# Performance work log

Measured on AMD Instinct MI355X. Metric: run time of the kernel, lower is better.

Reference implementation:

```python
import jax, jax.numpy as jnp
import numpy as np

B = 32768
NUM_SPARSE = 26
VOCAB = 100000
EMB = 128
DENSE_IN = 13
N_FIELDS = NUM_SPARSE + 1  # 27
INTER_DIM = N_FIELDS * (N_FIELDS - 1) // 2  # 351
TOP_IN = EMB + INTER_DIM  # 479


def setup_inputs() -> dict:
    key = jax.random.key(0)
    ks = jax.random.split(key, 12)
    inp = {
        "dense_x": jax.random.normal(ks[0], (B, DENSE_IN), dtype=jnp.float32),
        "sparse_x": jax.random.randint(ks[1], (B, NUM_SPARSE), 0, VOCAB, dtype=jnp.int64),
        # embedding tables stacked: [F, V, D]
        "emb_tables": jax.random.normal(ks[2], (NUM_SPARSE, VOCAB, EMB), dtype=jnp.float32) * 0.02,
        # bottom MLP: dense_in -> 256 -> emb
        "bw1": jax.random.normal(ks[3], (DENSE_IN, 256), dtype=jnp.float32) * 0.1,
        "bb1": jnp.zeros((256,), dtype=jnp.float32),
        "bw2": jax.random.normal(ks[4], (256, EMB), dtype=jnp.float32) * 0.05,
        "bb2": jnp.zeros((EMB,), dtype=jnp.float32),
        # top MLP: top_in -> 128 -> 64 -> 1
        "tw1": jax.random.normal(ks[5], (TOP_IN, 128), dtype=jnp.float32) * 0.05,
        "tb1": jnp.zeros((128,), dtype=jnp.float32),
        "tw2": jax.random.normal(ks[6], (128, 64), dtype=jnp.float32) * 0.1,
        "tb2": jnp.zeros((64,), dtype=jnp.float32),
        "tw3": jax.random.normal(ks[7], (64, 1), dtype=jnp.float32) * 0.1,
        "tb3": jnp.zeros((1,), dtype=jnp.float32),
    }
    return inp


def reference(dense_x, sparse_x, emb_tables, bw1, bb1, bw2, bb2,
              tw1, tb1, tw2, tb2, tw3, tb3):
    # bottom MLP
    h = jax.nn.relu(dense_x @ bw1 + bb1)
    x_bottom = jax.nn.relu(h @ bw2 + bb2)  # [B, EMB]

    # multi-table embedding gather: [B, F_sparse, EMB]
    field_idx = jnp.arange(NUM_SPARSE)[None, :]  # [1, F]
    sparse_embs = emb_tables[field_idx, sparse_x]  # [B, F, EMB]

    combined = jnp.concatenate([x_bottom[:, None, :], sparse_embs], axis=1)  # [B, 27, EMB]

    # pairwise dot interactions, take strict upper triangle
    interactions = jnp.einsum("bfd,bgd->bfg", combined, combined)  # [B, 27, 27]
    rows, cols = np.triu_indices(N_FIELDS, k=1)
    x_int = interactions[:, rows, cols]  # [B, 351]

    x_final = jnp.concatenate([x_bottom, x_int], axis=-1)  # [B, 479]

    # top MLP
    t = jax.nn.relu(x_final @ tw1 + tb1)
    t = jax.nn.relu(t @ tw2 + tb2)
    logits = t @ tw3 + tb3  # [B, 1]
    return jax.nn.sigmoid(logits)
```

## Files before the change

### kernel.cpp

```cpp
#include <hip/hip_runtime.h>
#include <hip/hip_bf16.h>
#include <stdint.h>

#define NUM_SPARSE 26
#define VOCAB 100000
#define EMB 128
#define ROWS 32

typedef __attribute__((ext_vector_type(8))) short bf16x8;
typedef __attribute__((ext_vector_type(16))) float f32x16;

__device__ __forceinline__ unsigned short f2bf(float x) {
    union { float f; uint32_t u; } v; v.f = x;
    uint32_t u = v.u;
    return (unsigned short)((u + 0x7FFFu + ((u >> 16) & 1u)) >> 16);
}
__device__ __forceinline__ uint32_t pack2bf(float a, float b) {
    return (uint32_t)f2bf(a) | ((uint32_t)f2bf(b) << 16);
}

__device__ __forceinline__ int swz(int r, int c, int rowbytes) {
    int b = 2 * c;
    return r * rowbytes + (((b >> 4) ^ (r & 15)) << 4) + (b & 15);
}
__device__ __forceinline__ bf16x8 ldsA(const char* base, int m, int k0, int rowbytes) {
    int slot = (k0 >> 3) ^ (m & 15);
    return *(const bf16x8*)(base + m * rowbytes + slot * 16);
}

__global__ void prep_weights(const float* __restrict__ bw2, const float* __restrict__ tw1,
                             const float* __restrict__ tw2, unsigned short* __restrict__ ws) {
    int i = blockIdx.x * blockDim.x + threadIdx.x;
    if (i < 128 * 256) {
        int n = i >> 8, k = i & 255;
        ws[i] = f2bf(bw2[k * 128 + n]);
    } else if (i < 128 * 256 + 128 * 480) {
        int j = i - 128 * 256;
        int n = j / 480, k = j - n * 480;
        ws[i] = f2bf(k < 479 ? tw1[k * 128 + n] : 0.f);
    } else if (i < 128 * 256 + 128 * 480 + 64 * 128) {
        int j = i - (128 * 256 + 128 * 480);
        int n = j >> 7, k = j & 127;
        ws[i] = f2bf(tw2[k * 64 + n]);
    }
}

__global__ __launch_bounds__(256, 2) void dlrm_main(
    const float* __restrict__ dense, const int* __restrict__ sparse,
    const float* __restrict__ emb, const float* __restrict__ bw1,
    const float* __restrict__ bb1, const float* __restrict__ bb2,
    const float* __restrict__ tb1, const float* __restrict__ tb2,
    const float* __restrict__ tw3, const float* __restrict__ tb3,
    const unsigned short* __restrict__ wsw, float* __restrict__ out)
{
    __shared__ __align__(16) char smem[65536];
    const int t = threadIdx.x;
    const int w = t >> 6;
    const int l = t & 63;
    const int hi = l >> 5;
    const int lm = l & 31;
    const int r0 = blockIdx.x * ROWS;

    float* xd = (float*)smem;
    char* xf = smem + 32768;

    for (int i = t; i < ROWS * 13; i += 256) xd[i] = dense[r0 * 13 + i];
    for (int i = t; i < ROWS * 33; i += 256) {
        int r = i / 33, c = 479 + (i - r * 33);
        *(unsigned short*)(xf + swz(r, c, 1024)) = 0;
    }
    __syncthreads();

    {
        char* hb = smem + 2048;
        int j = t;
        float w1r[13];
#pragma unroll
        for (int k = 0; k < 13; k++) w1r[k] = bw1[k * 256 + j];
        float b = bb1[j];
        for (int r = 0; r < ROWS; r++) {
            float acc = b;
#pragma unroll
            for (int k = 0; k < 13; k++) acc += xd[r * 13 + k] * w1r[k];
            *(unsigned short*)(hb + swz(r, j, 512)) = f2bf(fmaxf(acc, 0.f));
        }
    }
    __syncthreads();

    {
        const char* hb = smem + 2048;
        const unsigned short* bw2t = wsw;
        int n0 = w * 32;
        f32x16 acc = {0,0,0,0,0,0,0,0,0,0,0,0,0,0,0,0};
#pragma unroll
        for (int kk = 0; kk < 16; kk++) {
            int k0 = kk * 16 + hi * 8;
            bf16x8 a = ldsA(hb, lm, k0, 512);
            bf16x8 b = *(const bf16x8*)(bw2t + (n0 + lm) * 256 + k0);
            acc = __builtin_amdgcn_mfma_f32_32x32x16_bf16(a, b, acc, 0, 0, 0);
        }
        float bias = bb2[n0 + lm];
#pragma unroll
        for (int reg = 0; reg < 16; reg++) {
            int m = (reg & 3) + 8 * (reg >> 2) + 4 * hi;
            float v = fmaxf(acc[reg] + bias, 0.f);
            *(unsigned short*)(xf + swz(m, n0 + lm, 1024)) = f2bf(v);
        }
    }
    __syncthreads();

    {
        char* Cb = smem + w * 8192;
        for (int ri = 0; ri < 8; ri++) {
            int r = w * 8 + ri;
            int myidx = (l < NUM_SPARSE) ? sparse[(size_t)(r0 + r) * NUM_SPARSE + l] : 0;
            {
                uint32_t v = *(const uint32_t*)(xf + swz(r, 2 * l, 1024));
                *(uint32_t*)(Cb + 4 * l) = v;
            }
            float4 buf[13];
#pragma unroll
            for (int i = 0; i < 13; i++) {
                int fld = 2 * i + hi;
                int idx = __shfl(myidx, fld);
                buf[i] = *(const float4*)(emb + ((size_t)fld * VOCAB + (size_t)idx) * EMB + 4 * lm);
            }
#pragma unroll
            for (int i = 0; i < 13; i++) {
                int frow = 1 + 2 * i + hi;
                uint32_t p0 = pack2bf(buf[i].x, buf[i].y);
                uint32_t p1 = pack2bf(buf[i].z, buf[i].w);
                char* dst = Cb + frow * 256 + ((((lm >> 1) ^ (frow & 15))) << 4) + (lm & 1) * 8;
                *(uint32_t*)dst = p0;
                *(uint32_t*)(dst + 4) = p1;
            }
            f32x16 acc = {0,0,0,0,0,0,0,0,0,0,0,0,0,0,0,0};
#pragma unroll
            for (int kk = 0; kk < 8; kk++) {
                int k0 = kk * 16 + hi * 8;
                bf16x8 a = ldsA(Cb, lm, k0, 256);
                acc = __builtin_amdgcn_mfma_f32_32x32x16_bf16(a, a, acc, 0, 0, 0);
            }
            int n = lm;
            if (n >= 1 && n <= 26) {
#pragma unroll
                for (int reg = 0; reg < 16; reg++) {
                    int m = (reg & 3) + 8 * (reg >> 2) + 4 * hi;
                    if (m < n) {
                        int p = 26 * m - (m * (m - 1)) / 2 + (n - m - 1);
                        *(unsigned short*)(xf + swz(r, 128 + p, 1024)) = f2bf(acc[reg]);
                    }
                }
            }
        }
    }
    __syncthreads();

    {
        const unsigned short* tw1t = wsw + 32768;
        int n0 = w * 32;
        f32x16 acc = {0,0,0,0,0,0,0,0,0,0,0,0,0,0,0,0};
#pragma unroll
        for (int kk = 0; kk < 30; kk++) {
            int k0 = kk * 16 + hi * 8;
            bf16x8 a = ldsA(xf, lm, k0, 1024);
            bf16x8 b = *(const bf16x8*)(tw1t + (n0 + lm) * 480 + k0);
            acc = __builtin_amdgcn_mfma_f32_32x32x16_bf16(a, b, acc, 0, 0, 0);
        }
        float bias = tb1[n0 + lm];
#pragma unroll
        for (int reg = 0; reg < 16; reg++) {
            int m = (reg & 3) + 8 * (reg >> 2) + 4 * hi;
            float v = fmaxf(acc[reg] + bias, 0.f);
            *(unsigned short*)(smem + swz(m, n0 + lm, 256)) = f2bf(v);
        }
    }
    __syncthreads();

    float* t2b = (float*)(smem + 8192);
    if (w < 2) {
        const unsigned short* tw2t = wsw + 32768 + 61440;
        int n0 = w * 32;
        f32x16 acc = {0,0,0,0,0,0,0,0,0,0,0,0,0,0,0,0};
#pragma unroll
        for (int kk = 0; kk < 8; kk++) {
            int k0 = kk * 16 + hi * 8;
            bf16x8 a = ldsA(smem, lm, k0, 256);
            bf16x8 b = *(const bf16x8*)(tw2t + (n0 + lm) * 128 + k0);
            acc = __builtin_amdgcn_mfma_f32_32x32x16_bf16(a, b, acc, 0, 0, 0);
        }
        float bias = tb2[n0 + lm];
#pragma unroll
        for (int reg = 0; reg < 16; reg++) {
            int m = (reg & 3) + 8 * (reg >> 2) + 4 * hi;
            t2b[m * 65 + n0 + lm] = fmaxf(acc[reg] + bias, 0.f);
        }
    }
    __syncthreads();

    if (t < ROWS) {
        float acc = tb3[0];
#pragma unroll
        for (int k = 0; k < 64; k++) acc += t2b[t * 65 + k] * tw3[k];
        out[r0 + t] = 1.f / (1.f + expf(-acc));
    }
}

extern "C" void kernel_launch(void* const* d_in, const int* in_sizes, int n_in,
                              void* d_out, int out_size, void* d_ws, size_t ws_size,
                              hipStream_t stream) {
    const float* dense = (const float*)d_in[0];
    const int*   sparse = (const int*)d_in[1];
    const float* emb   = (const float*)d_in[2];
    const float* bw1   = (const float*)d_in[3];
    const float* bb1   = (const float*)d_in[4];
    const float* bw2   = (const float*)d_in[5];
    const float* bb2   = (const float*)d_in[6];
    const float* tw1   = (const float*)d_in[7];
    const float* tb1   = (const float*)d_in[8];
    const float* tw2   = (const float*)d_in[9];
    const float* tb2   = (const float*)d_in[10];
    const float* tw3   = (const float*)d_in[11];
    const float* tb3   = (const float*)d_in[12];
    unsigned short* wsw = (unsigned short*)d_ws;
    float* out = (float*)d_out;

    hipLaunchKernelGGL(prep_weights, dim3(400), dim3(256), 0, stream, bw2, tw1, tw2, wsw);
    hipLaunchKernelGGL(dlrm_main, dim3(32768 / ROWS), dim3(256), 0, stream,
                       dense, sparse, emb, bw1, bb1, bb2, tb1, tb2, tw3, tb3, wsw, out);
}
```

Baseline: 102.3 us.

## Software-pipeline embedding gathers with triple buffering and prefetch before bottom MLP

Preloads all eight sparse indices per wave up front, starts the embedding gathers for the first two rows before the bottom MLP, and triple-buffers the float4 gather registers so each row's gather is issued two rows ahead of its interaction MFMA. This is meant to hide global-memory gather latency behind the bottom MLP and the interaction compute. It also switches bf16 packing to the HIP intrinsic. The cost is much higher register pressure (39 float4 buffers) under launch_bounds(256,2), which could cause spills or lower occupancy.

Result: slower. 112.7 us (+10.2%).

```diff
diff --git a/kernel.cpp b/kernel.cpp
--- a/kernel.cpp
+++ b/kernel.cpp
@@ -16,7 +16,9 @@
     return (unsigned short)((u + 0x7FFFu + ((u >> 16) & 1u)) >> 16);
 }
 __device__ __forceinline__ uint32_t pack2bf(float a, float b) {
-    return (uint32_t)f2bf(a) | ((uint32_t)f2bf(b) << 16);
+    __hip_bfloat162 h2 = __float22bfloat162_rn(float2{a, b});
+    union { __hip_bfloat162 h; uint32_t u; } v; v.h = h2;
+    return v.u;
 }
 
 __device__ __forceinline__ int swz(int r, int c, int rowbytes) {
@@ -44,6 +46,50 @@
         ws[i] = f2bf(tw2[k * 64 + n]);
     }
 }
+
+#define GATHER(row, BUF)                                                               \
+    {                                                                                  \
+        _Pragma("unroll") for (int i = 0; i < 13; i++) {                               \
+            int fld = 2 * i + hi;                                                      \
+            int idx = __shfl(idxs[row], fld);                                          \
+            BUF[i] = *(const float4*)(emb + ((size_t)fld * VOCAB + (size_t)idx) * EMB  \
+                                      + 4 * lm);                                       \
+        }                                                                              \
+    }
+
+#define CONSUME(ri, BUF)                                                               \
+    {                                                                                  \
+        int r = w * 8 + (ri);                                                          \
+        {                                                                              \
+            uint32_t v = *(const uint32_t*)(xf + swz(r, 2 * l, 1024));                 \
+            *(uint32_t*)(Cb + 4 * l) = v;     \
+        }                                                                              \
+        _Pragma("unroll") for (int i = 0; i < 13; i++) {                               \
+            int frow = 1 + 2 * i + hi;                                                 \
+            uint32_t p0 = pack2bf(BUF[i].x, BUF[i].y);                                 \
+            uint32_t p1 = pack2bf(BUF[i].z, BUF[i].w);                                 \
+            char* dst = Cb + frow * 256 + ((((lm >> 1) ^ (frow & 15))) << 4)           \
+                        + (lm & 1) * 8;                                                \
+            *(uint32_t*)dst = p0;                                                      \
+            *(uint32_t*)(dst + 4) = p1;                                                \
+        }                                                                              \
+        f32x16 acc = {0,0,0,0,0,0,0,0,0,0,0,0,0,0,0,0};                                \
+        _Pragma("unroll") for (int kk = 0; kk < 8; kk++) {                             \
+            int k0 = kk * 16 + hi * 8;                                                 \
+            bf16x8 a = ldsA(Cb, lm, k0, 256);                                          \
+            acc = __builtin_amdgcn_mfma_f32_32x32x16_bf16(a, a, acc, 0, 0, 0);         \
+        }                                                                              \
+        int n = lm;                                                                    \
+        if (n >= 1 && n <= 26) {                                                       \
+            _Pragma("unroll") for (int reg = 0; reg < 16; reg++) {                     \
+                int m = (reg & 3) + 8 * (reg >> 2) + 4 * hi;                           \
+                if (m < n) {                                                           \
+                    int p = 26 * m - (m * (m - 1)) / 2 + (n - m - 1);                  \
+                    *(unsigned short*)(xf + swz(r, 128 + p, 1024)) = f2bf(acc[reg]);   \
+                }                                                                      \
+            }                                                                          \
+        }                                                                              \
+    }
 
 __global__ __launch_bounds__(256, 2) void dlrm_main(
     const float* __restrict__ dense, const int* __restrict__ sparse,
@@ -63,12 +109,23 @@
 
     float* xd = (float*)smem;
     char* xf = smem + 32768;
+    char* Cb = smem + w * 8192;
+
+    int idxs[8];
+#pragma unroll
+    for (int ri = 0; ri < 8; ri++)
+        idxs[ri] = (l < NUM_SPARSE)
+            ? sparse[(size_t)(r0 + w * 8 + ri) * NUM_SPARSE + l] : 0;
 
     for (int i = t; i < ROWS * 13; i += 256) xd[i] = dense[r0 * 13 + i];
     for (int i = t; i < ROWS * 33; i += 256) {
         int r = i / 33, c = 479 + (i - r * 33);
         *(unsigned short*)(xf + swz(r, c, 1024)) = 0;
     }
+
+    float4 bufA[13], bufB[13], bufC[13];
+    GATHER(0, bufA);
+    GATHER(1, bufB);
     __syncthreads();
 
     {
@@ -109,51 +166,14 @@
     }
     __syncthreads();
 
-    {
-        char* Cb = smem + w * 8192;
-        for (int ri = 0; ri < 8; ri++) {
-            int r = w * 8 + ri;
-            int myidx = (l < NUM_SPARSE) ? sparse[(size_t)(r0 + r) * NUM_SPARSE + l] : 0;
-            {
-                uint32_t v = *(const uint32_t*)(xf + swz(r, 2 * l, 1024));
-                *(uint32_t*)(Cb + 4 * l) = v;
-            }
-            float4 buf[13];
-#pragma unroll
-            for (int i = 0; i < 13; i++) {
-                int fld = 2 * i + hi;
-                int idx = __shfl(myidx, fld);
-                buf[i] = *(const float4*)(emb + ((size_t)fld * VOCAB + (size_t)idx) * EMB + 4 * lm);
-            }
-#pragma unroll
-            for (int i = 0; i < 13; i++) {
-                int frow = 1 + 2 * i + hi;
-                uint32_t p0 = pack2bf(buf[i].x, buf[i].y);
-                uint32_t p1 = pack2bf(buf[i].z, buf[i].w);
-                char* dst = Cb + frow * 256 + ((((lm >> 1) ^ (frow & 15))) << 4) + (lm & 1) * 8;
-                *(uint32_t*)dst = p0;
-                *(uint32_t*)(dst + 4) = p1;
-            }
-            f32x16 acc = {0,0,0,0,0,0,0,0,0,0,0,0,0,0,0,0};
-#pragma unroll
-            for (int kk = 0; kk < 8; kk++) {
-                int k0 = kk * 16 + hi * 8;
-                bf16x8 a = ldsA(Cb, lm, k0, 256);
-                acc = __builtin_amdgcn_mfma_f32_32x32x16_bf16(a, a, acc, 0, 0, 0);
-            }
-            int n = lm;
-            if (n >= 1 && n <= 26) {
-#pragma unroll
-                for (int reg = 0; reg < 16; reg++) {
-                    int m = (reg & 3) + 8 * (reg >> 2) + 4 * hi;
-                    if (m < n) {
-                        int p = 26 * m - (m * (m - 1)) / 2 + (n - m - 1);
-                        *(unsigned short*)(xf + swz(r, 128 + p, 1024)) = f2bf(acc[reg]);
-                    }
-                }
-            }
-        }
-    }
+    GATHER(2, bufC); CONSUME(0, bufA);
+    GATHER(3, bufA); CONSUME(1, bufB);
+    GATHER(4, bufB); CONSUME(2, bufC);
+    GATHER(5, bufC); CONSUME(3, bufA);
+    GATHER(6, bufA); CONSUME(4, bufB);
+    GATHER(7, bufB); CONSUME(5, bufC);
+    CONSUME(6, bufA);
+    CONSUME(7, bufB);
     __syncthreads();
 
     {
```
